# Optimization experiments

Hardware: AMD Instinct MI355X
Metric: run time of the kernel (lower is better)

Reference implementation:

```python
import jax, jax.numpy as jnp
import numpy as np

B, CIN, NH, W, L, K = 16, 64, 64, 32, 4, 5
EPS = 1e-5
FORGET_BIAS = 1.0


def conv(x, w, b=None):
    # x: [B,C,H,W], w: [O,I,k,k] -> SAME padding, stride 1 (NCHW)
    y = jax.lax.conv_general_dilated(x, w, (1, 1), 'SAME',
                                     dimension_numbers=('NCHW', 'OIHW', 'NCHW'))
    if b is not None:
        y = y + b[None, :, None, None]
    return y


def ln(x, g, b):
    # torch LayerNorm([C,W,W]): normalize each sample over (C,H,W)
    m = jnp.mean(x, axis=(1, 2, 3), keepdims=True)
    v = jnp.mean((x - m) ** 2, axis=(1, 2, 3), keepdims=True)
    return (x - m) * jax.lax.rsqrt(v + EPS) * g[None] + b[None]


def attn_channel(q, kv):
    # q: [B,C,W,H], kv: [B,L,C,W,H]
    b, c, w, h = q.shape
    qf = q.reshape(b, c, w * h)                 # [B,C,HW]
    kf = kv.reshape(b, -1, w * h)               # [B,L*C,HW]
    a = jax.nn.softmax(jnp.einsum('bcp,blp->bcl', qf, kf), axis=2)  # [B,C,L*C]
    out = jnp.einsum('bcl,blp->bcp', a, kf)     # [B,C,HW]
    return out.reshape(b, c, w, h)


def attn_spatial(q, kv):
    # q: [B,C,W,H], kv: [B,L,C,W,H]
    b, c, w, h = q.shape
    qf = q.reshape(b, c, w * h).transpose(0, 2, 1)          # [B,HW,C]
    kf = kv.transpose(0, 1, 3, 4, 2).reshape(b, -1, c)      # [B,L*HW,C]
    a = jax.nn.softmax(jnp.einsum('bpc,bqc->bpq', qf, kf), axis=2)  # [B,HW,L*HW]
    out = jnp.einsum('bpq,bqc->bpc', a, kf)                 # [B,HW,C]
    return out.reshape(b, w, h, c).transpose(0, 3, 1, 2)


def setup_inputs() -> dict:
    key = jax.random.key(0)
    ks = iter(jax.random.split(key, 64))
    rn = lambda shape, s=1.0: jax.random.normal(next(ks), shape, jnp.float32) * s
    ones = lambda shape: jnp.ones(shape, jnp.float32)
    zeros = lambda shape: jnp.zeros(shape, jnp.float32)
    s = 0.02
    d = {}
    d['x_t'] = rn((B, CIN, W, W))
    d['h_t'] = rn((B, NH, W, W))
    d['c_t'] = rn((B, NH, W, W))
    d['c_historys'] = rn((B, L, NH, W, W))
    d['m_t'] = rn((B, NH, W, W))
    d['w_x'] = rn((7 * NH, CIN, K, K), s); d['ln_x_g'] = ones((7 * NH, W, W)); d['ln_x_b'] = zeros((7 * NH, W, W))
    d['w_h'] = rn((4 * NH, NH, K, K), s);  d['ln_h_g'] = ones((4 * NH, W, W)); d['ln_h_b'] = zeros((4 * NH, W, W))
    d['w_m'] = rn((3 * NH, NH, K, K), s);  d['ln_m_g'] = ones((3 * NH, W, W)); d['ln_m_b'] = zeros((3 * NH, W, W))
    d['w_o'] = rn((NH, 2 * NH, K, K), s);  d['ln_o_g'] = ones((NH, W, W));     d['ln_o_b'] = zeros((NH, W, W))
    d['w_last'] = rn((NH, 2 * NH, 1, 1), s)
    d['s_norm_g'] = ones((NH, W, W)); d['s_norm_b'] = zeros((NH, W, W))
    d['c_norm_g'] = ones((NH, W, W)); d['c_norm_b'] = zeros((NH, W, W))
    d['ca_w1'] = rn((NH, NH, K, K), s); d['ca_b1'] = zeros((NH,))
    d['ca_ln_g'] = ones((NH, W, W));    d['ca_ln_b'] = zeros((NH, W, W))
    d['ca_w2'] = rn((NH, NH, 1, 1), s); d['ca_b2'] = zeros((NH,))
    d['sa_w1'] = rn((NH, NH, K, K), s)
    d['sa_ln_g'] = ones((NH, W, W));    d['sa_ln_b'] = zeros((NH, W, W))
    d['sa_w2'] = rn((NH, NH, 1, 1), s)
    d['attn_w'] = rn((NH, NH, 1, 1), s)
    return d


def reference(x_t, h_t, c_t, c_historys, m_t,
              w_x, ln_x_g, ln_x_b, w_h, ln_h_g, ln_h_b, w_m, ln_m_g, ln_m_b,
              w_o, ln_o_g, ln_o_b, w_last,
              s_norm_g, s_norm_b, c_norm_g, c_norm_b,
              ca_w1, ca_b1, ca_ln_g, ca_ln_b, ca_w2, ca_b2,
              sa_w1, sa_ln_g, sa_ln_b, sa_w2, attn_w):
    x_concat = ln(conv(x_t, w_x), ln_x_g, ln_x_b)
    h_concat = ln(conv(h_t, w_h), ln_h_g, ln_h_b)
    m_concat = ln(conv(m_t, w_m), ln_m_g, ln_m_b)
    (i_x, f_x, g_x, i_xp, f_xp, g_xp, o_x) = jnp.split(x_concat, 7, axis=1)
    (i_h, f_h, g_h, o_h) = jnp.split(h_concat, 4, axis=1)
    (i_m, f_m, g_m) = jnp.split(m_concat, 3, axis=1)

    i_t = jax.nn.sigmoid(i_x + i_h)
    f_t = jax.nn.sigmoid(f_x + f_h + FORGET_BIAS)
    g_t = jnp.tanh(g_x + g_h)

    # attn_sum_fussion(c_t, query=f_t, keys=c_historys, values=c_historys)
    sp = ln(c_t + attn_spatial(f_t, c_historys), s_norm_g, s_norm_b)
    ch = ln(c_t + attn_channel(f_t, c_historys), c_norm_g, c_norm_b)
    s_a = conv(jax.nn.relu(ln(conv(sp, sa_w1), sa_ln_g, sa_ln_b)), sa_w2)
    c_a = conv(jax.nn.relu(ln(conv(ch, ca_w1, ca_b1), ca_ln_g, ca_ln_b)), ca_w2, ca_b2)
    attn = conv(s_a + c_a, attn_w)
    c_new = attn + i_t * g_t

    i_tp = jax.nn.sigmoid(i_xp + i_m)
    f_tp = jax.nn.sigmoid(f_xp + f_m + FORGET_BIAS)
    g_tp = jnp.tanh(g_xp + g_m)
    m_new = f_tp * m_t + i_tp * g_tp

    mem = jnp.concatenate((c_new, m_new), axis=1)
    o_t = jax.nn.sigmoid(o_x + o_h + ln(conv(mem, w_o), ln_o_g, ln_o_b))
    h_new = o_t * jnp.tanh(conv(mem, w_last))
    return h_new, c_new, m_new
```

## Files before the change

kernel.cpp:

```cpp
#include <hip/hip_runtime.h>
#include <hip/hip_bf16.h>

#define N1 (1u << 20)

typedef __attribute__((ext_vector_type(8))) short s8v;
typedef __attribute__((ext_vector_type(4))) float f4v;

static __device__ __forceinline__ float sigm(float x){ return 1.f/(1.f + __expf(-x)); }
static __device__ __forceinline__ float tanh_(float x){ return 1.f - 2.f/(__expf(2.f*x) + 1.f); }

static __device__ __forceinline__ ushort f2b(float f){
  union { float f; uint u; } x; x.f = f;
  uint r = x.u + 0x7FFFu + ((x.u >> 16) & 1u);
  return (ushort)(r >> 16);
}

static __device__ __forceinline__ void red_atomic2(float s, float q, float* d, int b, int t){
  #pragma unroll
  for (int m = 32; m; m >>= 1){ s += __shfl_xor(s, m); q += __shfl_xor(q, m); }
  if ((t & 63) == 0){ atomicAdd(&d[b*2], s); atomicAdd(&d[b*2+1], q); }
}

__global__ __launch_bounds__(256) void k_pre(
    const float* __restrict__ wX, ushort* __restrict__ dX,
    const float* __restrict__ wH, ushort* __restrict__ dH,
    const float* __restrict__ wM, ushort* __restrict__ dM,
    const float* __restrict__ x_t, ushort* __restrict__ xT,
    const float* __restrict__ h_t, ushort* __restrict__ hT,
    const float* __restrict__ m_t, ushort* __restrict__ mT,
    float* __restrict__ zs)
{
  const int bid = blockIdx.x, t = threadIdx.x;
  __shared__ __align__(16) float T[64][68];
  if (bid < 5600){
    if (bid == 0) zs[t] = 0.f;
    int idx = bid*256 + t;
    const float* s; ushort* d; int Co;
    if (idx < 716800){ s=wX; d=dX; Co=448; }
    else if ((idx -= 716800) < 409600){ s=wH; d=dH; Co=256; }
    else if ((idx -= 409600) < 307200){ s=wM; d=dM; Co=192; }
    else return;
    int ci = idx & 63; int r = idx >> 6; int co = r % Co; int tap = r / Co;
    d[idx] = f2b(s[((size_t)(co*64 + ci))*25 + tap]);
    return;
  }
  const int j = bid - 5600;
  const int p0 = (j & 15) << 6;
  const int lp = j >> 4;
  const float* src; ushort* outT; int pl;
  if (lp < 16){ src = x_t; outT = xT; pl = lp; }
  else if (lp < 32){ src = h_t; outT = hT; pl = lp - 16; }
  else { src = m_t; outT = mT; pl = lp - 32; }
  const float* sp = src + ((size_t)pl << 16);
  const int c = t >> 2, g = t & 3;
  #pragma unroll
  for (int i = 0; i < 4; ++i)
    *(float4*)&T[c][(g<<4)+(i<<2)] = *(const float4*)(sp + ((size_t)c << 10) + p0 + (g<<4) + (i<<2));
  __syncthreads();
  const int p = t >> 2, c0 = (t & 3) << 4;
  uint w4[8];
  #pragma unroll
  for (int k = 0; k < 8; ++k)
    w4[k] = (uint)f2b(T[c0+2*k][p]) | ((uint)f2b(T[c0+2*k+1][p]) << 16);
  ushort* dst = outT + ((((size_t)pl << 10) + p0 + p) << 6) + c0;
  *(uint4*)(dst)     = *(uint4*)&w4[0];
  *(uint4*)(dst + 8) = *(uint4*)&w4[4];
}

__global__ __launch_bounds__(256) void k_postgates(
    const float* __restrict__ wO, ushort* __restrict__ dO,
    const float* __restrict__ wSA, ushort* __restrict__ dSA,
    const float* __restrict__ wCA, ushort* __restrict__ dCA,
    const float* __restrict__ chist, ushort* __restrict__ kvC, ushort* __restrict__ kvT,
    const float* __restrict__ ft, ushort* __restrict__ ftC, ushort* __restrict__ qT,
    const float* __restrict__ memo, ushort* __restrict__ memoT)
{
  const int bid = blockIdx.x, t = threadIdx.x;
  __shared__ __align__(16) float T[64][68];
  if (bid < 1600){
    int idx = bid*256 + t;
    const float* s; ushort* d; int Co, Ci;
    if (idx < 204800){ s=wO; d=dO; Co=64; Ci=128; }
    else if ((idx -= 204800) < 102400){ s=wSA; d=dSA; Co=64; Ci=64; }
    else if ((idx -= 102400) < 102400){ s=wCA; d=dCA; Co=64; Ci=64; }
    else return;
    int ci = idx % Ci; int r = idx / Ci; int co = r % Co; int tap = r / Co;
    d[idx] = f2b(s[((size_t)(co*Ci + ci))*25 + tap]);
    return;
  }
  const int j = bid - 1600;
  const int p0 = (j & 15) << 6;
  const int lp = j >> 4;
  const int c = t >> 2, g = t & 3;
  if (lp < 80){
    const float* src; ushort* outC; ushort* outT; int pl;
    if (lp < 64){ src = chist; outC = kvC; outT = kvT; pl = lp; }
    else { src = ft; outC = ftC; outT = qT; pl = lp - 64; }
    const float* sp = src + ((size_t)pl << 16);
    #pragma unroll
    for (int i = 0; i < 4; ++i){
      float4 f = *(const float4*)(sp + ((size_t)c << 10) + p0 + (g<<4) + (i<<2));
      *(float4*)&T[c][(g<<4)+(i<<2)] = f;
      uint2 pk2;
      pk2.x = (uint)f2b(f.x) | ((uint)f2b(f.y) << 16);
      pk2.y = (uint)f2b(f.z) | ((uint)f2b(f.w) << 16);
      *(uint2*)(outC + ((((size_t)pl << 6) + c) << 10) + p0 + (g<<4) + (i<<2)) = pk2;
    }
    __syncthreads();
    const int p = t >> 2, c0 = (t & 3) << 4;
    uint w4[8];
    #pragma unroll
    for (int k = 0; k < 8; ++k)
      w4[k] = (uint)f2b(T[c0+2*k][p]) | ((uint)f2b(T[c0+2*k+1][p]) << 16);
    ushort* dst = outT + ((((size_t)pl << 10) + p0 + p) << 6) + c0;
    *(uint4*)(dst)     = *(uint4*)&w4[0];
    *(uint4*)(dst + 8) = *(uint4*)&w4[4];
  } else {
    const int b = lp - 80;
    const float* sp = memo + ((size_t)(b*2 + 1) << 16);
    #pragma unroll
    for (int i = 0; i < 4; ++i)
      *(float4*)&T[c][(g<<4)+(i<<2)] = *(const float4*)(sp + ((size_t)c << 10) + p0 + (g<<4) + (i<<2));
    __syncthreads();
    const int p = t >> 2, c0 = (t & 3) << 4;
    uint w4[8];
    #pragma unroll
    for (int k = 0; k < 8; ++k)
      w4[k] = (uint)f2b(T[c0+2*k][p]) | ((uint)f2b(T[c0+2*k+1][p]) << 16);
    ushort* dst = memoT + ((((size_t)b << 10) + p0 + p) << 7) + 64 + c0;
    *(uint4*)(dst)     = *(uint4*)&w4[0];
    *(uint4*)(dst + 8) = *(uint4*)&w4[4];
  }
}

struct PT { const float* s; ushort* d; const float* st; const float* g; const float* bb; };

__global__ __launch_bounds__(256) void k_prepT3(PT ja, PT jb, PT jc, int n0, int n1, float invN)
{
  const int lp = blockIdx.y;
  PT j; int pl;
  if (lp < n0){ j = ja; pl = lp; }
  else if (lp < n0 + n1){ j = jb; pl = lp - n0; }
  else { j = jc; pl = lp - n0 - n1; }
  const float* sp = j.s + ((size_t)pl << 16);
  float mean = 0.f, rstd = 0.f;
  if (j.st){
    float s0 = j.st[pl*2], s1 = j.st[pl*2+1];
    mean = s0*invN; rstd = rsqrtf(s1*invN - mean*mean + 1e-5f);
  }
  const int p0 = blockIdx.x << 6;
  __shared__ __align__(16) float T[64][68];
  const int t = threadIdx.x, c = t >> 2, g4 = t & 3;
  #pragma unroll
  for (int i = 0; i < 4; ++i){
    const int px = (g4 << 4) + (i << 2);
    float4 f = *(const float4*)(sp + ((size_t)c << 10) + p0 + px);
    if (j.st){
      const size_t li = ((size_t)c << 10) + p0 + px;
      float4 gv = *(const float4*)(j.g + li);
      float4 bv = *(const float4*)(j.bb + li);
      f.x = (f.x - mean)*rstd*gv.x + bv.x;
      f.y = (f.y - mean)*rstd*gv.y + bv.y;
      f.z = (f.z - mean)*rstd*gv.z + bv.z;
      f.w = (f.w - mean)*rstd*gv.w + bv.w;
    }
    *(float4*)&T[c][px] = f;
  }
  __syncthreads();
  const int p = t >> 2, c0 = (t & 3) << 4;
  uint w4[8];
  #pragma unroll
  for (int k = 0; k < 8; ++k){
    ushort lo = f2b(T[c0 + 2*k][p]);
    ushort hi = f2b(T[c0 + 2*k + 1][p]);
    w4[k] = (uint)lo | ((uint)hi << 16);
  }
  ushort* dst = j.d + ((((size_t)pl << 10) + p0 + p) << 6) + c0;
  *(uint4*)(dst)     = *(uint4*)&w4[0];
  *(uint4*)(dst + 8) = *(uint4*)&w4[4];
}

struct Seg {
  const ushort* inT; const ushort* w; const float* bias;
  float* out; float* ostat;
  int Cin, Cout;
};
struct Segs3 { Seg s[3]; int b1, b2; };

template<int MT, int RPB>
__global__ __launch_bounds__(256, MT==4 ? 2 : 3) void k_convX(Segs3 Sg)
{
  constexpr int CO   = MT*16;
  constexpr int NW   = 5*CO*4;
  constexpr int ITW  = (NW + 255) / 256;
  constexpr int DXSH = (MT == 4 ? 8 : 7);
  constexpr int PXB  = 32/RPB;
  constexpr int ROWS = RPB + 4;
  constexpr int RPW  = RPB/4;
  constexpr int NTIL = RPB/2;
  constexpr int SUN2 = ROWS*36;

  const int b = blockIdx.y;
  const int cog = blockIdx.x / PXB, pxblk = blockIdx.x % PXB;
  const int si = (cog >= Sg.b1) + (cog >= Sg.b2);
  const Seg sg = Sg.s[si];
  const int base = si == 0 ? 0 : (si == 1 ? Sg.b1 : Sg.b2);
  const int co0 = (cog - base) * CO;
  const int r0 = pxblk * RPB;
  const int t = threadIdx.x, w = t >> 6, l = t & 63;
  const int lane16 = l & 15, quad = l >> 4;

  __shared__ __align__(16) ushort S_[4][ROWS][36][8];
  __shared__ __align__(16) ushort W_[2][5*CO*32];

  f4v acc[MT][NTIL];
  #pragma unroll
  for (int mi = 0; mi < MT; ++mi)
    #pragma unroll
    for (int n = 0; n < NTIL; ++n) acc[mi][n] = (f4v){0.f,0.f,0.f,0.f};

  size_t woff0[ITW];
  #pragma unroll
  for (int it = 0; it < ITW; ++it){
    const int u = t + it*256;
    const int l16u = u & 15, qu = (u >> 4) & 3;
    const int miu = (u >> 6) & (MT - 1), dxu = u >> DXSH;
    woff0[it] = ((size_t)(dxu*sg.Cout + co0 + miu*16 + l16u))*sg.Cin + (qu << 3);
  }
  const size_t wdy = (size_t)5 * sg.Cout * sg.Cin;

  const int ncc = sg.Cin >> 5;
  for (int cc = 0; cc < ncc; ++cc){
    __syncthreads();
    for (int idx = t; idx < SUN2; idx += 256){
      const int row = idx / 36, col = idx - row*36;
      const int ir = r0 - 2 + row, ic = col - 2;
      uint4 pk[4] = {make_uint4(0,0,0,0),make_uint4(0,0,0,0),make_uint4(0,0,0,0),make_uint4(0,0,0,0)};
      if ((unsigned)ir < 32u && (unsigned)ic < 32u){
        const ushort* bp = sg.inT + ((size_t)((b << 10) + (ir << 5) + ic)) * sg.Cin + (cc << 5);
        #pragma unroll
        for (int q = 0; q < 4; ++q) pk[q] = *(const uint4*)(bp + (q << 3));
      }
      #pragma unroll
      for (int q = 0; q < 4; ++q) *(uint4*)&S_[q][row][col][0] = pk[q];
    }
    {
      uint4 wreg[ITW];
      #pragma unroll
      for (int it = 0; it < ITW; ++it)
        if (ITW*256 == NW || t + it*256 < NW)
          wreg[it] = *(const uint4*)(sg.w + woff0[it] + (cc << 5));
      #pragma unroll
      for (int it = 0; it < ITW; ++it)
        if (ITW*256 == NW || t + it*256 < NW)
          *(uint4*)&W_[0][(size_t)(t + it*256) * 8] = wreg[it];
    }
    __syncthreads();
    #pragma unroll
    for (int dy = 0; dy < 5; ++dy){
      uint4 nreg[ITW];
      if (dy < 4){
        #pragma unroll
        for (int it = 0; it < ITW; ++it)
          if (ITW*256 == NW || t + it*256 < NW)
            nreg[it] = *(const uint4*)(sg.w + woff0[it] + (size_t)(dy+1)*wdy + (cc << 5));
      }
      #pragma unroll
      for (int dx = 0; dx < 5; ++dx){
        s8v a[MT];
        #pragma unroll
        for (int mi = 0; mi < MT; ++mi){
          const int au = ((((dx*MT + mi) << 2) + quad) << 4) + lane16;
          a[mi] = *(const s8v*)&W_[dy & 1][au << 3];
        }
        #pragma unroll
        for (int n = 0; n < NTIL; ++n){
          const int srow = w*RPW + (n >> 1) + dy;
          const int col = ((n & 1) << 4) + lane16 + dx;
          s8v bb = *(const s8v*)&S_[quad][srow][col][0];
          #pragma unroll
          for (int mi = 0; mi < MT; ++mi)
            acc[mi][n] = __builtin_amdgcn_mfma_f32_16x16x32_bf16(a[mi], bb, acc[mi][n], 0, 0, 0);
        }
      }
      if (dy < 4){
        #pragma unroll
        for (int it = 0; it < ITW; ++it)
          if (ITW*256 == NW || t + it*256 < NW)
            *(uint4*)&W_[(dy+1) & 1][(size_t)(t + it*256) * 8] = nreg[it];
      }
      __syncthreads();
    }
  }
  float lsum = 0.f, lsq = 0.f;
  #pragma unroll
  for (int mi = 0; mi < MT; ++mi){
    const int co = co0 + mi*16 + (quad << 2);
    #pragma unroll
    for (int n = 0; n < NTIL; ++n){
      const int row = r0 + w*RPW + (n >> 1);
      const int col = ((n & 1) << 4) + lane16;
      #pragma unroll
      for (int i = 0; i < 4; ++i){
        float v = acc[mi][n][i] + (sg.bias ? sg.bias[co+i] : 0.f);
        sg.out[(((size_t)(b*sg.Cout + co + i)) << 10) + (row << 5) + col] = v;
        lsum += v; lsq += v*v;
      }
    }
  }
  if (sg.ostat) red_atomic2(lsum, lsq, sg.ostat, b, t);
}

__global__ __launch_bounds__(256) void k_gates(
    const float* __restrict__ bufx, const float* __restrict__ bufh, const float* __restrict__ bufm,
    const float* __restrict__ lnxg, const float* __restrict__ lnxb,
    const float* __restrict__ lnhg, const float* __restrict__ lnhb,
    const float* __restrict__ lnmg, const float* __restrict__ lnmb,
    const float* __restrict__ m_t, const float* __restrict__ stats,
    float* __restrict__ ft, float* __restrict__ ig, float* __restrict__ osum,
    float* __restrict__ memo, float* __restrict__ out_m)
{
  const int idx = blockIdx.x*256 + threadIdx.x;
  const int b = idx >> 16, rem = idx & 65535;
  const int c = rem >> 10, p = rem & 1023;

  float mx = stats[b*2]      * (1.f/458752.f);
  float vx = stats[b*2+1]    * (1.f/458752.f) - mx*mx;  float rx = rsqrtf(vx + 1e-5f);
  float mh = stats[32+b*2]   * (1.f/262144.f);
  float vh = stats[32+b*2+1] * (1.f/262144.f) - mh*mh;  float rh = rsqrtf(vh + 1e-5f);
  float mm = stats[64+b*2]   * (1.f/196608.f);
  float vm = stats[64+b*2+1] * (1.f/196608.f) - mm*mm;  float rm = rsqrtf(vm + 1e-5f);

  auto LX = [&](int k){
    size_t ch = (size_t)k*64 + c; size_t gi = ((size_t)b*448 + ch)*1024 + p; size_t li = ch*1024 + p;
    return (bufx[gi] - mx)*rx*lnxg[li] + lnxb[li]; };
  auto LH = [&](int k){
    size_t ch = (size_t)k*64 + c; size_t gi = ((size_t)b*256 + ch)*1024 + p; size_t li = ch*1024 + p;
    return (bufh[gi] - mh)*rh*lnhg[li] + lnhb[li]; };
  auto LM = [&](int k){
    size_t ch = (size_t)k*64 + c; size_t gi = ((size_t)b*192 + ch)*1024 + p; size_t li = ch*1024 + p;
    return (bufm[gi] - mm)*rm*lnmg[li] + lnmb[li]; };

  float i_t = sigm(LX(0) + LH(0));
  float f_t = sigm(LX(1) + LH(1) + 1.f);
  float g_t = tanh_(LX(2) + LH(2));
  float i_p = sigm(LX(3) + LM(0));
  float f_p = sigm(LX(4) + LM(1) + 1.f);
  float g_p = tanh_(LX(5) + LM(2));
  float ox = LX(6), oh = LH(3);

  ft[idx]   = f_t;
  ig[idx]   = i_t * g_t;
  osum[idx] = ox + oh;
  float mn = f_p * m_t[idx] + i_p * g_p;
  out_m[idx] = mn;
  memo[((size_t)(b*128 + 64 + c) << 10) + p] = mn;
}

__global__ __launch_bounds__(256) void k_spat_chlog(
    const ushort* __restrict__ qT, const ushort* __restrict__ kvC, const ushort* __restrict__ kvT,
    float* __restrict__ num, float* __restrict__ den,
    const ushort* __restrict__ ftC, float* __restrict__ lg)
{
  __shared__ __align__(16) char smem[44288];
  const int bid = blockIdx.x, t = threadIdx.x;
  const int w = t >> 6, l = t & 63;
  const int lane16 = l & 15, quad = l >> 4;

  if (bid < 512){
    const int p0 = (bid & 15) << 6, b = (bid >> 4) & 15, half = bid >> 8;
    ushort (*Kt)[72] = reinterpret_cast<ushort(*)[72]>(smem);
    ushort (*Kc)[72] = reinterpret_cast<ushort(*)[72]>(smem + 9216);
    ushort (*Eb)[72] = reinterpret_cast<ushort(*)[72]>(smem + 18432);
    float  (*XO)[65] = reinterpret_cast<float(*)[65]>(smem + 27648);

    s8v qa0, qa1;
    {
      const ushort* qr = qT + ((((size_t)b << 10) + p0 + (w << 4) + lane16) << 6) + (quad << 3);
      qa0 = *(const s8v*)(qr);
      qa1 = *(const s8v*)(qr + 32);
    }
    f4v o0 = {0.f,0.f,0.f,0.f}, o1 = o0, o2 = o0, o3 = o0, dacc = o0;
    const short oneb = (short)0x3F80;
    const s8v ones = { oneb, oneb, oneb, oneb, oneb, oneb, oneb, oneb };

    const int r = t >> 2, g4 = (t & 3) << 4;
    for (int ck = 0; ck < 32; ++ck){
      const int chunk = (half << 5) + ck;
      const int lidx = chunk >> 4, pk = (chunk & 15) << 6;
      __syncthreads();
      {
        const ushort* sc = kvC + ((((size_t)(b*4 + lidx) << 6) + r) << 10) + pk + g4;
        *(uint4*)&Kc[r][g4]     = *(const uint4*)(sc);
        *(uint4*)&Kc[r][g4 + 8] = *(const uint4*)(sc + 8);
        const ushort* st = kvT + ((((size_t)(b*4 + lidx) << 10) + pk + r) << 6) + g4;
        *(uint4*)&Kt[r][g4]     = *(const uint4*)(st);
        *(uint4*)&Kt[r][g4 + 8] = *(const uint4*)(st + 8);
      }
      __syncthreads();
      #pragma unroll
      for (int nt = 0; nt < 4; ++nt){
        const ushort* bt = &Kt[(nt << 4) + lane16][quad << 3];
        s8v b0 = *(const s8v*)(bt);
        s8v b1 = *(const s8v*)(bt + 32);
        f4v s = {0.f,0.f,0.f,0.f};
        s = __builtin_amdgcn_mfma_f32_16x16x32_bf16(qa0, b0, s, 0, 0, 0);
        s = __builtin_amdgcn_mfma_f32_16x16x32_bf16(qa1, b1, s, 0, 0, 0);
        #pragma unroll
        for (int i = 0; i < 4; ++i){
          float e = __expf(s[i] - 12.f);
          Eb[(w << 4) + (quad << 2) + i][(nt << 4) + lane16] = f2b(e);
        }
      }
      __syncthreads();
      #pragma unroll
      for (int ks = 0; ks < 2; ++ks){
        s8v ea = *(const s8v*)&Eb[(w << 4) + lane16][(ks << 5) + (quad << 3)];
        dacc = __builtin_amdgcn_mfma_f32_16x16x32_bf16(ea, ones, dacc, 0, 0, 0);
        s8v bc0 = *(const s8v*)&Kc[ 0 + lane16][(ks << 5) + (quad << 3)];
        s8v bc1 = *(const s8v*)&Kc[16 + lane16][(ks << 5) + (quad << 3)];
        s8v bc2 = *(const s8v*)&Kc[32 + lane16][(ks << 5) + (quad << 3)];
        s8v bc3 = *(const s8v*)&Kc[48 + lane16][(ks << 5) + (quad << 3)];
        o0 = __builtin_amdgcn_mfma_f32_16x16x32_bf16(ea, bc0, o0, 0, 0, 0);
        o1 = __builtin_amdgcn_mfma_f32_16x16x32_bf16(ea, bc1, o1, 0, 0, 0);
        o2 = __builtin_amdgcn_mfma_f32_16x16x32_bf16(ea, bc2, o2, 0, 0, 0);
        o3 = __builtin_amdgcn_mfma_f32_16x16x32_bf16(ea, bc3, o3, 0, 0, 0);
      }
    }
    {
      const int pxl = (w << 4) + (quad << 2);
      if (lane16 == 0){
        float* dp = den + (((size_t)(half*16 + b)) << 10) + p0 + pxl;
        dp[0] = dacc[0]; dp[1] = dacc[1]; dp[2] = dacc[2]; dp[3] = dacc[3];
      }
      XO[ 0 + lane16][pxl+0] = o0[0]; XO[ 0 + lane16][pxl+1] = o0[1];
      XO[ 0 + lane16][pxl+2] = o0[2]; XO[ 0 + lane16][pxl+3] = o0[3];
      XO[16 + lane16][pxl+0] = o1[0]; XO[16 + lane16][pxl+1] = o1[1];
      XO[16 + lane16][pxl+2] = o1[2]; XO[16 + lane16][pxl+3] = o1[3];
      XO[32 + lane16][pxl+0] = o2[0]; XO[32 + lane16][pxl+1] = o2[1];
      XO[32 + lane16][pxl+2] = o2[2]; XO[32 + lane16][pxl+3] = o2[3];
      XO[48 + lane16][pxl+0] = o3[0]; XO[48 + lane16][pxl+1] = o3[1];
      XO[48 + lane16][pxl+2] = o3[2]; XO[48 + lane16][pxl+3] = o3[3];
    }
    __syncthreads();
    {
      const int ch = t >> 2;
      float* nout = num + (size_t)half * N1;
      #pragma unroll
      for (int i = 0; i < 4; ++i){
        size_t gi = ((size_t)b << 16) + ((size_t)ch << 10) + p0 + g4 + (i << 2);
        float4 ov;
        ov.x = XO[ch][g4 + (i << 2) + 0];
        ov.y = XO[ch][g4 + (i << 2) + 1];
        ov.z = XO[ch][g4 + (i << 2) + 2];
        ov.w = XO[ch][g4 + (i << 2) + 3];
        *(float4*)(nout + gi) = ov;
      }
    }
  } else {
    const int j = bid - 512;
    const int bx = j & 7, b = j >> 3;
    const int np = bx >> 1, mp = bx & 1;
    ushort (*As)[32][8] = reinterpret_cast<ushort(*)[32][8]>(smem);
    ushort (*Bs)[64][8] = reinterpret_cast<ushort(*)[64][8]>(smem + 4096);
    f4v acc[2];
    acc[0] = (f4v){0.f,0.f,0.f,0.f}; acc[1] = (f4v){0.f,0.f,0.f,0.f};

    for (int kc = 0; kc < 16; ++kc){
      __syncthreads();
      {
        const int c = t >> 3, q = t & 7;
        *(uint4*)&As[q][c][0] = *(const uint4*)(ftC + (((size_t)(b*64 + mp*32 + c)) << 10) + (kc<<6) + (q<<3));
      }
      #pragma unroll
      for (int it = 0; it < 2; ++it){
        const int idx = t + it*256;
        const int r2 = idx >> 3, q = idx & 7;
        *(uint4*)&Bs[q][r2][0] = *(const uint4*)(kvC + ((((size_t)(b*4 + np) << 6) + r2) << 10) + (kc<<6) + (q<<3));
      }
      __syncthreads();
      #pragma unroll
      for (int ks = 0; ks < 2; ++ks){
        s8v a0 = *(const s8v*)&As[(ks<<2)+quad][lane16][0];
        s8v a1 = *(const s8v*)&As[(ks<<2)+quad][16 + lane16][0];
        s8v bb = *(const s8v*)&Bs[(ks<<2)+quad][(w<<4) + lane16][0];
        acc[0] = __builtin_amdgcn_mfma_f32_16x16x32_bf16(a0, bb, acc[0], 0, 0, 0);
        acc[1] = __builtin_amdgcn_mfma_f32_16x16x32_bf16(a1, bb, acc[1], 0, 0, 0);
      }
    }
    #pragma unroll
    for (int mi = 0; mi < 2; ++mi)
      #pragma unroll
      for (int i = 0; i < 4; ++i){
        const int c = mp*32 + mi*16 + (quad<<2) + i;
        const int n = (np<<6) + (w<<4) + lane16;
        lg[(((size_t)(b*64 + c)) << 8) + n] = acc[mi][i];
      }
  }
}

__global__ __launch_bounds__(256) void k_chsm_spcomb(
    const float* __restrict__ a, ushort* __restrict__ ab,
    const float* __restrict__ num, const float* __restrict__ den,
    const float* __restrict__ c_t, float* __restrict__ sp_raw, float* __restrict__ stats)
{
  const int bid = blockIdx.x, t = threadIdx.x;
  if (bid < 256){
    const int row  = bid*4 + (t >> 6);
    const int lane = t & 63;
    const float* rp = a + ((size_t)row << 8);
    float v0 = rp[lane], v1 = rp[lane+64], v2 = rp[lane+128], v3 = rp[lane+192];
    float mx = fmaxf(fmaxf(v0, v1), fmaxf(v2, v3));
    #pragma unroll
    for (int m = 32; m; m >>= 1) mx = fmaxf(mx, __shfl_xor(mx, m));
    v0 = __expf(v0 - mx); v1 = __expf(v1 - mx); v2 = __expf(v2 - mx); v3 = __expf(v3 - mx);
    float s = v0 + v1 + v2 + v3;
    #pragma unroll
    for (int m = 32; m; m >>= 1) s += __shfl_xor(s, m);
    float inv = 1.f / s;
    ushort* op = ab + ((size_t)row << 8);
    op[lane] = f2b(v0*inv); op[lane+64] = f2b(v1*inv);
    op[lane+128] = f2b(v2*inv); op[lane+192] = f2b(v3*inv);
  } else {
    const int j = bid - 256;
    const int p0 = (j & 15) << 6, b = j >> 4;
    const int ch = t >> 2, g4 = (t & 3) << 4;
    float lsum = 0.f, lsq = 0.f;
    #pragma unroll
    for (int i = 0; i < 4; ++i){
      const int px = p0 + g4 + (i << 2);
      size_t gi = ((size_t)b << 16) + ((size_t)ch << 10) + px;
      float4 n0 = *(const float4*)(num + gi);
      float4 n1 = *(const float4*)(num + (size_t)N1 + gi);
      const float* d0 = den + (((size_t)b) << 10) + px;
      const float* d1 = den + (((size_t)(16 + b)) << 10) + px;
      float4 cv = *(const float4*)(c_t + gi);
      float4 ov;
      ov.x = cv.x + (n0.x + n1.x) / (d0[0] + d1[0]);
      ov.y = cv.y + (n0.y + n1.y) / (d0[1] + d1[1]);
      ov.z = cv.z + (n0.z + n1.z) / (d0[2] + d1[2]);
      ov.w = cv.w + (n0.w + n1.w) / (d0[3] + d1[3]);
      *(float4*)(sp_raw + gi) = ov;
      lsum += ov.x + ov.y + ov.z + ov.w;
      lsq  += ov.x*ov.x + ov.y*ov.y + ov.z*ov.z + ov.w*ov.w;
    }
    red_atomic2(lsum, lsq, stats, b, t);
  }
}

__global__ __launch_bounds__(256) void k_chout_m(
    const ushort* __restrict__ chlb, const ushort* __restrict__ kvT,
    const float* __restrict__ c_t, float* __restrict__ ch_raw, float* __restrict__ stats)
{
  const int p0 = blockIdx.x << 6, b = blockIdx.y;
  const int t = threadIdx.x, w = t >> 6, l = t & 63;
  const int lane16 = l & 15, quad = l >> 4;
  __shared__ __align__(16) ushort As[32][64][8];
  __shared__ __align__(16) ushort Bs[32][32][8];
  #pragma unroll
  for (int it = 0; it < 8; ++it){
    const int idx = t + it*256;
    const int c = idx >> 5, q = idx & 31;
    *(uint4*)&As[q][c][0] = *(const uint4*)(chlb + (((size_t)(b*64 + c)) << 8) + (q<<3));
  }
  __syncthreads();
  s8v a[8];
  #pragma unroll
  for (int ks = 0; ks < 8; ++ks)
    a[ks] = *(const s8v*)&As[(ks<<2)+quad][(w<<4) + lane16][0];
  float lsum = 0.f, lsq = 0.f;
  for (int pc = 0; pc < 2; ++pc){
    __syncthreads();
    #pragma unroll
    for (int it = 0; it < 4; ++it){
      const int idx = t + it*256;
      const int px = idx >> 5, q = idx & 31;
      const int plane = (b<<2) + (q>>3);
      *(uint4*)&Bs[q][px][0] = *(const uint4*)(kvT + ((((size_t)plane << 10) + p0 + (pc<<5) + px) << 6) + ((q&7)<<3));
    }
    __syncthreads();
    #pragma unroll
    for (int nt = 0; nt < 2; ++nt){
      f4v o = {0.f,0.f,0.f,0.f};
      #pragma unroll
      for (int ks = 0; ks < 8; ++ks){
        s8v bb = *(const s8v*)&Bs[(ks<<2)+quad][(nt<<4) + lane16][0];
        o = __builtin_amdgcn_mfma_f32_16x16x32_bf16(a[ks], bb, o, 0, 0, 0);
      }
      #pragma unroll
      for (int i = 0; i < 4; ++i){
        const int c = (w<<4) + (quad<<2) + i;
        const int px = p0 + (pc<<5) + (nt<<4) + lane16;
        size_t gi = ((size_t)b << 16) + ((size_t)c << 10) + px;
        float v = c_t[gi] + o[i];
        ch_raw[gi] = v;
        lsum += v; lsq += v*v;
      }
    }
  }
  red_atomic2(lsum, lsq, stats, b, t);
}

__global__ __launch_bounds__(256) void k_attnfinal(
    const float* __restrict__ samid, const float* __restrict__ camid,
    const float* __restrict__ stats_sa, const float* __restrict__ stats_ca,
    const float* __restrict__ salng, const float* __restrict__ salnb,
    const float* __restrict__ calng, const float* __restrict__ calnb,
    const float* __restrict__ wsa2, const float* __restrict__ wca2,
    const float* __restrict__ cab2, const float* __restrict__ wat,
    const float* __restrict__ ig, float* __restrict__ out_c, float* __restrict__ memo,
    ushort* __restrict__ memoT)
{
  const int p0 = blockIdx.x << 6, b = blockIdx.y, t = threadIdx.x;
  const int tc = t & 15, tp = t >> 4;
  __shared__ __align__(16) float R[64][68];
  __shared__ __align__(16) float Wl[64][68];
  __shared__ __align__(16) float Ms[64][68];
  const float invN = 1.f/65536.f;
  float acc[4][4] = {};
  #pragma unroll
  for (int pass = 0; pass < 2; ++pass){
    const float* mid = pass ? camid : samid;
    const float* st  = pass ? stats_ca : stats_sa;
    const float* g   = pass ? calng : salng;
    const float* bb  = pass ? calnb : salnb;
    const float* w   = pass ? wca2  : wsa2;
    float mean = st[b*2]*invN;
    float var  = st[b*2+1]*invN - mean*mean;
    float rstd = rsqrtf(var + 1e-5f);
    __syncthreads();
    {
      const int j = t & 63, c0 = t >> 6;
      for (int ci = c0; ci < 64; ci += 4){
        size_t gi = ((size_t)b << 16) + ((size_t)ci << 10) + p0 + j;
        size_t li = ((size_t)ci << 10) + p0 + j;
        float v = (mid[gi] - mean)*rstd*g[li] + bb[li];
        R[ci][j] = fmaxf(v, 0.f);
      }
      const int ci2 = t & 63, c20 = t >> 6;
      for (int c2 = c20; c2 < 64; c2 += 4) Wl[ci2][c2] = w[((size_t)c2 << 6) + ci2];
    }
    __syncthreads();
    for (int ci = 0; ci < 64; ++ci){
      float wv[4], rv[4];
      *(float4*)wv = *(const float4*)&Wl[ci][4*tc];
      *(float4*)rv = *(const float4*)&R[ci][4*tp];
      #pragma unroll
      for (int i = 0; i < 4; ++i)
        #pragma unroll
        for (int j = 0; j < 4; ++j)
          acc[i][j] = fmaf(wv[i], rv[j], acc[i][j]);
    }
  }
  {
    float b2[4];
    #pragma unroll
    for (int i = 0; i < 4; ++i) b2[i] = cab2[4*tc + i];
    #pragma unroll
    for (int i = 0; i < 4; ++i)
      #pragma unroll
      for (int j = 0; j < 4; ++j)
        Ms[4*tc+i][4*tp+j] = acc[i][j] + b2[i];
  }
  __syncthreads();
  {
    const int ci2 = t & 63, c20 = t >> 6;
    for (int c2 = c20; c2 < 64; c2 += 4) Wl[ci2][c2] = wat[((size_t)c2 << 6) + ci2];
  }
  __syncthreads();
  float acc2[4][4] = {};
  for (int c2 = 0; c2 < 64; ++c2){
    float wv[4], mv[4];
    *(float4*)wv = *(const float4*)&Wl[c2][4*tc];
    *(float4*)mv = *(const float4*)&Ms[c2][4*tp];
    #pragma unroll
    for (int i = 0; i < 4; ++i)
      #pragma unroll
      for (int j = 0; j < 4; ++j)
        acc2[i][j] = fmaf(wv[i], mv[j], acc2[i][j]);
  }
  float vv[4][4];
  #pragma unroll
  for (int i = 0; i < 4; ++i)
    #pragma unroll
    for (int j = 0; j < 4; ++j){
      size_t gi = ((size_t)b << 16) + ((size_t)(4*tc + i) << 10) + p0 + 4*tp + j;
      float v = acc2[i][j] + ig[gi];
      vv[i][j] = v;
      out_c[gi] = v;
      memo[((size_t)(b*128 + 4*tc + i) << 10) + p0 + 4*tp + j] = v;
    }
  #pragma unroll
  for (int j = 0; j < 4; ++j){
    uint2 pk;
    pk.x = (uint)f2b(vv[0][j]) | ((uint)f2b(vv[1][j]) << 16);
    pk.y = (uint)f2b(vv[2][j]) | ((uint)f2b(vv[3][j]) << 16);
    *(uint2*)(memoT + ((((size_t)b << 10) + p0 + 4*tp + j) << 7) + 4*tc) = pk;
  }
}

__global__ __launch_bounds__(256) void k_final(
    const float* __restrict__ memo, const float* __restrict__ wlast,
    const float* __restrict__ bufo, const float* __restrict__ osum,
    const float* __restrict__ stats_o, const float* __restrict__ lnog, const float* __restrict__ lnob,
    float* __restrict__ out_h)
{
  const int p0 = blockIdx.x << 6, b = blockIdx.y, t = threadIdx.x;
  const int tc = t & 15, tp = t >> 4;
  __shared__ __align__(16) float Msh[64][68];
  __shared__ __align__(16) float Wt[64][68];
  float acc[4][4] = {};
  #pragma unroll
  for (int half = 0; half < 2; ++half){
    __syncthreads();
    {
      const int j = t & 63, c0 = t >> 6;
      for (int ci = c0; ci < 64; ci += 4)
        Msh[ci][j] = memo[((size_t)(b*128 + half*64 + ci) << 10) + p0 + j];
      const int ci2 = t & 63, co0 = t >> 6;
      for (int co = co0; co < 64; co += 4) Wt[ci2][co] = wlast[((size_t)co << 7) + half*64 + ci2];
    }
    __syncthreads();
    for (int ci = 0; ci < 64; ++ci){
      float wv[4], mv[4];
      *(float4*)wv = *(const float4*)&Wt[ci][4*tc];
      *(float4*)mv = *(const float4*)&Msh[ci][4*tp];
      #pragma unroll
      for (int i = 0; i < 4; ++i)
        #pragma unroll
        for (int j = 0; j < 4; ++j)
          acc[i][j] = fmaf(wv[i], mv[j], acc[i][j]);
    }
  }
  float mean = stats_o[b*2]*(1.f/65536.f);
  float var  = stats_o[b*2+1]*(1.f/65536.f) - mean*mean;
  float rstd = rsqrtf(var + 1e-5f);
  #pragma unroll
  for (int i = 0; i < 4; ++i)
    #pragma unroll
    for (int j = 0; j < 4; ++j){
      const int co = 4*tc + i, p = p0 + 4*tp + j;
      size_t gi = ((size_t)b << 16) + ((size_t)co << 10) + p;
      size_t li = ((size_t)co << 10) + p;
      float lno = (bufo[gi] - mean)*rstd*lnog[li] + lnob[li];
      float o = sigm(osum[gi] + lno);
      out_h[gi] = o * tanh_(acc[i][j]);
    }
}

extern "C" void kernel_launch(void* const* d_in, const int* in_sizes, int n_in,
                              void* d_out, int out_size, void* d_ws, size_t ws_size,
                              hipStream_t stream)
{
  const float* x_t   = (const float*)d_in[0];
  const float* h_t   = (const float*)d_in[1];
  const float* c_t   = (const float*)d_in[2];
  const float* chist = (const float*)d_in[3];
  const float* m_t   = (const float*)d_in[4];
  const float* w_x   = (const float*)d_in[5];
  const float* lnxg  = (const float*)d_in[6];
  const float* lnxb  = (const float*)d_in[7];
  const float* w_h   = (const float*)d_in[8];
  const float* lnhg  = (const float*)d_in[9];
  const float* lnhb  = (const float*)d_in[10];
  const float* w_m   = (const float*)d_in[11];
  const float* lnmg  = (const float*)d_in[12];
  const float* lnmb  = (const float*)d_in[13];
  const float* w_o   = (const float*)d_in[14];
  const float* lnog  = (const float*)d_in[15];
  const float* lnob  = (const float*)d_in[16];
  const float* w_last= (const float*)d_in[17];
  const float* sng   = (const float*)d_in[18];
  const float* snb   = (const float*)d_in[19];
  const float* cng   = (const float*)d_in[20];
  const float* cnb   = (const float*)d_in[21];
  const float* ca_w1 = (const float*)d_in[22];
  const float* ca_b1 = (const float*)d_in[23];
  const float* calng = (const float*)d_in[24];
  const float* calnb = (const float*)d_in[25];
  const float* ca_w2 = (const float*)d_in[26];
  const float* ca_b2 = (const float*)d_in[27];
  const float* sa_w1 = (const float*)d_in[28];
  const float* salng = (const float*)d_in[29];
  const float* salnb = (const float*)d_in[30];
  const float* sa_w2 = (const float*)d_in[31];
  const float* attn_w= (const float*)d_in[32];

  float* out = (float*)d_out;
  float* ws  = (float*)d_ws;

  float* stats = ws;
  float* bufx  = ws + 1024;
  float* bufh  = bufx + 7*(size_t)N1;
  float* bufm  = bufh + 4*(size_t)N1;
  float* ft    = bufm + 3*(size_t)N1;
  float* ig    = ft   + (size_t)N1;
  float* osum  = ig   + (size_t)N1;
  float* memo  = osum + (size_t)N1;
  float* sp    = bufx;
  float* ch    = bufx + (size_t)N1;
  float* samid = bufx + 2*(size_t)N1;
  float* camid = bufx + 3*(size_t)N1;
  float* bufo  = bufx + 4*(size_t)N1;
  float* chl   = bufx + 5*(size_t)N1;
  ushort* kvC  = (ushort*)bufh;
  ushort* kvT  = kvC + 4*(size_t)N1;
  ushort* qT   = (ushort*)bufm;
  ushort* ftC  = qT + (size_t)N1;

  ushort* xT   = (ushort*)memo;
  ushort* hT   = xT + (size_t)N1;
  ushort* mT   = hT + (size_t)N1;
  ushort* spT  = ftC + (size_t)N1;
  ushort* chT  = spT + (size_t)N1;
  ushort* memoT = chT + (size_t)N1;
  float*  numB = bufx;

  ushort* wbx = (ushort*)ft;
  ushort* wbh = wbx + 716800;
  ushort* wbm = wbh + 409600;
  ushort* wbo  = (ushort*)(chl + 262144);
  ushort* wbsa = wbo + 204800;
  ushort* wbca = wbsa + 102400;
  ushort* chlb = wbca + 102400;
  float*  denP = chl + 600000;

  float* out_h = out;
  float* out_c = out + (size_t)N1;
  float* out_m = out + 2*(size_t)N1;

  k_pre<<<dim3(6368), dim3(256), 0, stream>>>(w_x, wbx, w_h, wbh, w_m, wbm,
                                              x_t, xT, h_t, hT, m_t, mT, stats);

  {
    Segs3 XHM;
    XHM.s[0] = Seg{ xT, wbx, nullptr, bufx, stats+0,  64, 448 };
    XHM.s[1] = Seg{ hT, wbh, nullptr, bufh, stats+32, 64, 256 };
    XHM.s[2] = Seg{ mT, wbm, nullptr, bufm, stats+64, 64, 192 };
    XHM.b1 = 7; XHM.b2 = 11;
    k_convX<4,8><<<dim3(56,16), dim3(256), 0, stream>>>(XHM);
  }

  k_gates<<<dim3(4096), dim3(256), 0, stream>>>(bufx, bufh, bufm, lnxg, lnxb, lnhg, lnhb,
                                                lnmg, lnmb, m_t, stats,
                                                ft, ig, osum, memo, out_m);

  k_postgates<<<dim3(3136), dim3(256), 0, stream>>>(w_o, wbo, sa_w1, wbsa, ca_w1, wbca,
                                                    chist, kvC, kvT, ft, ftC, qT,
                                                    memo, memoT);

  k_spat_chlog<<<dim3(640), dim3(256), 0, stream>>>(qT, kvC, kvT, numB, denP, ftC, chl);

  k_chsm_spcomb<<<dim3(512), dim3(256), 0, stream>>>(chl, chlb, numB, denP, c_t, sp, stats+96);

  k_chout_m<<<dim3(16,16), dim3(256), 0, stream>>>(chlb, kvT, c_t, ch, stats+128);

  {
    PT js{ sp, spT, stats+96,  sng, snb };
    PT jc{ ch, chT, stats+128, cng, cnb };
    k_prepT3<<<dim3(16,32), dim3(256), 0, stream>>>(js, jc, js, 16, 16, 1.f/65536.f);
  }

  {
    Segs3 SC;
    SC.s[0] = Seg{ spT, wbsa, nullptr, samid, stats+160, 64, 64 };
    SC.s[1] = Seg{ chT, wbca, ca_b1,   camid, stats+192, 64, 64 };
    SC.s[2] = SC.s[1];
    SC.b1 = 2; SC.b2 = 1000;
    k_convX<2,8><<<dim3(16,16), dim3(256), 0, stream>>>(SC);
  }

  k_attnfinal<<<dim3(16,16), dim3(256), 0, stream>>>(samid, camid, stats+160, stats+192,
                                                     salng, salnb, calng, calnb,
                                                     sa_w2, ca_w2, ca_b2, attn_w,
                                                     ig, out_c, memo, memoT);

  {
    Segs3 O;
    O.s[0] = Seg{ memoT, wbo, nullptr, bufo, stats+224, 128, 64 };
    O.s[1] = O.s[0]; O.s[2] = O.s[0];
    O.b1 = 1000; O.b2 = 1000;
    k_convX<2,8><<<dim3(8,16), dim3(256), 0, stream>>>(O);
  }

  k_final<<<dim3(16,16), dim3(256), 0, stream>>>(memo, w_last, bufo, osum, stats+224,
                                                 lnog, lnob, out_h);
}
```

Measured before the change: 471.2 us.

## Repack weights and activations into conv-tile-contiguous blocked layouts

```diff
diff --git a/kernel.cpp b/kernel.cpp
--- a/kernel.cpp
+++ b/kernel.cpp
@@ -19,6 +19,24 @@
   #pragma unroll
   for (int m = 32; m; m >>= 1){ s += __shfl_xor(s, m); q += __shfl_xor(q, m); }
   if ((t & 63) == 0){ atomicAdd(&d[b*2], s); atomicAdd(&d[b*2+1], q); }
+}
+
+static __device__ __forceinline__ void wpack1(const float* __restrict__ s,
+                                              ushort* __restrict__ d,
+                                              int idx, int Co, int Ci, int CO)
+{
+  const int MTl = CO >> 4;
+  const int NWl = 20*CO;
+  const int nCot = Co / CO;
+  int e = idx & 7; int r = idx >> 3;
+  int u = r % NWl; r /= NWl;
+  int cot = r % nCot; r /= nCot;
+  int dy = r % 5; int cc = r / 5;
+  int l16 = u & 15, q = (u >> 4) & 3, t2 = u >> 6;
+  int mi = t2 % MTl, dx = t2 / MTl;
+  int co = cot*CO + mi*16 + l16;
+  int ci = (cc << 5) + (q << 3) + e;
+  d[idx] = f2b(s[((size_t)(co*Ci + ci))*25 + dy*5 + dx]);
 }
 
 __global__ __launch_bounds__(256) void k_pre(
@@ -35,13 +53,9 @@
   if (bid < 5600){
     if (bid == 0) zs[t] = 0.f;
     int idx = bid*256 + t;
-    const float* s; ushort* d; int Co;
-    if (idx < 716800){ s=wX; d=dX; Co=448; }
-    else if ((idx -= 716800) < 409600){ s=wH; d=dH; Co=256; }
-    else if ((idx -= 409600) < 307200){ s=wM; d=dM; Co=192; }
-    else return;
-    int ci = idx & 63; int r = idx >> 6; int co = r % Co; int tap = r / Co;
-    d[idx] = f2b(s[((size_t)(co*64 + ci))*25 + tap]);
+    if (idx < 716800){ wpack1(wX, dX, idx, 448, 64, 64); }
+    else if ((idx -= 716800) < 409600){ wpack1(wH, dH, idx, 256, 64, 64); }
+    else if ((idx -= 409600) < 307200){ wpack1(wM, dM, idx, 192, 64, 64); }
     return;
   }
   const int j = bid - 5600;
@@ -62,9 +76,11 @@
   #pragma unroll
   for (int k = 0; k < 8; ++k)
     w4[k] = (uint)f2b(T[c0+2*k][p]) | ((uint)f2b(T[c0+2*k+1][p]) << 16);
-  ushort* dst = outT + ((((size_t)pl << 10) + p0 + p) << 6) + c0;
-  *(uint4*)(dst)     = *(uint4*)&w4[0];
-  *(uint4*)(dst + 8) = *(uint4*)&w4[4];
+  const int q0 = c0 >> 3;
+  ushort* d0 = outT + ((((size_t)pl*8 + q0    ) << 10) + p0 + p)*8;
+  ushort* d1 = outT + ((((size_t)pl*8 + q0 + 1) << 10) + p0 + p)*8;
+  *(uint4*)d0 = *(uint4*)&w4[0];
+  *(uint4*)d1 = *(uint4*)&w4[4];
 }
 
 __global__ __launch_bounds__(256) void k_postgates(
@@ -79,13 +95,9 @@
   __shared__ __align__(16) float T[64][68];
   if (bid < 1600){
     int idx = bid*256 + t;
-    const float* s; ushort* d; int Co, Ci;
-    if (idx < 204800){ s=wO; d=dO; Co=64; Ci=128; }
-    else if ((idx -= 204800) < 102400){ s=wSA; d=dSA; Co=64; Ci=64; }
-    else if ((idx -= 102400) < 102400){ s=wCA; d=dCA; Co=64; Ci=64; }
-    else return;
-    int ci = idx % Ci; int r = idx / Ci; int co = r % Co; int tap = r / Co;
-    d[idx] = f2b(s[((size_t)(co*Ci + ci))*25 + tap]);
+    if (idx < 204800){ wpack1(wO, dO, idx, 64, 128, 32); }
+    else if ((idx -= 204800) < 102400){ wpack1(wSA, dSA, idx, 64, 64, 32); }
+    else if ((idx -= 102400) < 102400){ wpack1(wCA, dCA, idx, 64, 64, 32); }
     return;
   }
   const int j = bid - 1600;
@@ -127,9 +139,11 @@
     #pragma unroll
     for (int k = 0; k < 8; ++k)
       w4[k] = (uint)f2b(T[c0+2*k][p]) | ((uint)f2b(T[c0+2*k+1][p]) << 16);
-    ushort* dst = memoT + ((((size_t)b << 10) + p0 + p) << 7) + 64 + c0;
-    *(uint4*)(dst)     = *(uint4*)&w4[0];
-    *(uint4*)(dst + 8) = *(uint4*)&w4[4];
+    const int q0 = 8 + (c0 >> 3);
+    ushort* d0 = memoT + ((((size_t)(b*16 + q0    )) << 10) + p0 + p)*8;
+    ushort* d1 = memoT + ((((size_t)(b*16 + q0 + 1)) << 10) + p0 + p)*8;
+    *(uint4*)d0 = *(uint4*)&w4[0];
+    *(uint4*)d1 = *(uint4*)&w4[4];
   }
 }
 
@@ -175,9 +189,11 @@
     ushort hi = f2b(T[c0 + 2*k + 1][p]);
     w4[k] = (uint)lo | ((uint)hi << 16);
   }
-  ushort* dst = j.d + ((((size_t)pl << 10) + p0 + p) << 6) + c0;
-  *(uint4*)(dst)     = *(uint4*)&w4[0];
-  *(uint4*)(dst + 8) = *(uint4*)&w4[4];
+  const int q0 = c0 >> 3;
+  ushort* d0 = j.d + ((((size_t)pl*8 + q0    ) << 10) + p0 + p)*8;
+  ushort* d1 = j.d + ((((size_t)pl*8 + q0 + 1) << 10) + p0 + p)*8;
+  *(uint4*)d0 = *(uint4*)&w4[0];
+  *(uint4*)d1 = *(uint4*)&w4[4];
 }
 
 struct Seg {
@@ -193,77 +209,72 @@
   constexpr int CO   = MT*16;
   constexpr int NW   = 5*CO*4;
   constexpr int ITW  = (NW + 255) / 256;
-  constexpr int DXSH = (MT == 4 ? 8 : 7);
   constexpr int PXB  = 32/RPB;
   constexpr int ROWS = RPB + 4;
   constexpr int RPW  = RPB/4;
   constexpr int NTIL = RPB/2;
-  constexpr int SUN2 = ROWS*36;
+  constexpr int SUN  = 4*ROWS*36;
 
   const int b = blockIdx.y;
   const int cog = blockIdx.x / PXB, pxblk = blockIdx.x % PXB;
   const int si = (cog >= Sg.b1) + (cog >= Sg.b2);
   const Seg sg = Sg.s[si];
   const int base = si == 0 ? 0 : (si == 1 ? Sg.b1 : Sg.b2);
-  const int co0 = (cog - base) * CO;
+  const int cot = cog - base;
+  const int co0 = cot * CO;
   const int r0 = pxblk * RPB;
   const int t = threadIdx.x, w = t >> 6, l = t & 63;
   const int lane16 = l & 15, quad = l >> 4;
+  const int nCot = sg.Cout / CO;
+  const int ngrp = sg.Cin >> 3;
 
   __shared__ __align__(16) ushort S_[4][ROWS][36][8];
-  __shared__ __align__(16) ushort W_[2][5*CO*32];
+  __shared__ __align__(16) ushort W_[2][NW*8];
 
   f4v acc[MT][NTIL];
   #pragma unroll
   for (int mi = 0; mi < MT; ++mi)
     #pragma unroll
     for (int n = 0; n < NTIL; ++n) acc[mi][n] = (f4v){0.f,0.f,0.f,0.f};
-
-  size_t woff0[ITW];
-  #pragma unroll
-  for (int it = 0; it < ITW; ++it){
-    const int u = t + it*256;
-    const int l16u = u & 15, qu = (u >> 4) & 3;
-    const int miu = (u >> 6) & (MT - 1), dxu = u >> DXSH;
-    woff0[it] = ((size_t)(dxu*sg.Cout + co0 + miu*16 + l16u))*sg.Cin + (qu << 3);
-  }
-  const size_t wdy = (size_t)5 * sg.Cout * sg.Cin;
 
   const int ncc = sg.Cin >> 5;
   for (int cc = 0; cc < ncc; ++cc){
     __syncthreads();
-    for (int idx = t; idx < SUN2; idx += 256){
-      const int row = idx / 36, col = idx - row*36;
+    for (int idx = t; idx < SUN; idx += 256){
+      const int q   = idx / (ROWS*36);
+      const int rem = idx - q*(ROWS*36);
+      const int row = rem / 36, col = rem - row*36;
       const int ir = r0 - 2 + row, ic = col - 2;
-      uint4 pk[4] = {make_uint4(0,0,0,0),make_uint4(0,0,0,0),make_uint4(0,0,0,0),make_uint4(0,0,0,0)};
-      if ((unsigned)ir < 32u && (unsigned)ic < 32u){
-        const ushort* bp = sg.inT + ((size_t)((b << 10) + (ir << 5) + ic)) * sg.Cin + (cc << 5);
-        #pragma unroll
-        for (int q = 0; q < 4; ++q) pk[q] = *(const uint4*)(bp + (q << 3));
-      }
-      #pragma unroll
-      for (int q = 0; q < 4; ++q) *(uint4*)&S_[q][row][col][0] = pk[q];
+      uint4 pk = make_uint4(0,0,0,0);
+      if ((unsigned)ir < 32u && (unsigned)ic < 32u)
+        pk = *(const uint4*)(sg.inT + ((((size_t)(b*ngrp + (cc<<2) + q)) << 10) + (ir<<5) + ic)*8);
+      *(uint4*)&S_[q][row][col][0] = pk;
     }
     {
+      const ushort* wb = sg.w + ((((size_t)(cc*5)*nCot + cot)*NW) << 3);
       uint4 wreg[ITW];
       #pragma unroll
-      for (int it = 0; it < ITW; ++it)
-        if (ITW*256 == NW || t + it*256 < NW)
-          wreg[it] = *(const uint4*)(sg.w + woff0[it] + (cc << 5));
-      #pragma unroll
-      for (int it = 0; it < ITW; ++it)
-        if (ITW*256 == NW || t + it*256 < NW)
-          *(uint4*)&W_[0][(size_t)(t + it*256) * 8] = wreg[it];
+      for (int it = 0; it < ITW; ++it){
+        const int u = t + it*256;
+        if (ITW*256 == NW || u < NW) wreg[it] = *(const uint4*)(wb + ((size_t)u << 3));
+      }
+      #pragma unroll
+      for (int it = 0; it < ITW; ++it){
+        const int u = t + it*256;
+        if (ITW*256 == NW || u < NW) *(uint4*)&W_[0][(size_t)u * 8] = wreg[it];
+      }
     }
     __syncthreads();
     #pragma unroll
     for (int dy = 0; dy < 5; ++dy){
       uint4 nreg[ITW];
       if (dy < 4){
+        const ushort* wbn = sg.w + ((((size_t)(cc*5 + dy + 1)*nCot + cot)*NW) << 3);
         #pragma unroll
-        for (int it = 0; it < ITW; ++it)
-          if (ITW*256 == NW || t + it*256 < NW)
-            nreg[it] = *(const uint4*)(sg.w + woff0[it] + (size_t)(dy+1)*wdy + (cc << 5));
+        for (int it = 0; it < ITW; ++it){
+          const int u = t + it*256;
+          if (ITW*256 == NW || u < NW) nreg[it] = *(const uint4*)(wbn + ((size_t)u << 3));
+        }
       }
       #pragma unroll
       for (int dx = 0; dx < 5; ++dx){
@@ -285,9 +296,10 @@
       }
       if (dy < 4){
         #pragma unroll
-        for (int it = 0; it < ITW; ++it)
-          if (ITW*256 == NW || t + it*256 < NW)
-            *(uint4*)&W_[(dy+1) & 1][(size_t)(t + it*256) * 8] = nreg[it];
+        for (int it = 0; it < ITW; ++it){
+          const int u = t + it*256;
+          if (ITW*256 == NW || u < NW) *(uint4*)&W_[(dy+1) & 1][(size_t)u * 8] = nreg[it];
+        }
       }
       __syncthreads();
     }
@@ -695,7 +707,8 @@
     uint2 pk;
     pk.x = (uint)f2b(vv[0][j]) | ((uint)f2b(vv[1][j]) << 16);
     pk.y = (uint)f2b(vv[2][j]) | ((uint)f2b(vv[3][j]) << 16);
-    *(uint2*)(memoT + ((((size_t)b << 10) + p0 + 4*tp + j) << 7) + 4*tc) = pk;
+    const int px = p0 + 4*tp + j;
+    *(uint2*)(memoT + ((((size_t)(b*16 + (tc >> 1))) << 10) + px)*8 + ((tc & 1) << 2)) = pk;
   }
 }
 
```

Result: no change. 476.0 us (+1.0%).

## Single-buffer conv weight tile with register prefetch to raise occupancy

Applied to the files above, without the earlier changes.

```diff
diff --git a/kernel.cpp b/kernel.cpp
--- a/kernel.cpp
+++ b/kernel.cpp
@@ -188,7 +188,7 @@
 struct Segs3 { Seg s[3]; int b1, b2; };
 
 template<int MT, int RPB>
-__global__ __launch_bounds__(256, MT==4 ? 2 : 3) void k_convX(Segs3 Sg)
+__global__ __launch_bounds__(256, MT==4 ? 3 : 4) void k_convX(Segs3 Sg)
 {
   constexpr int CO   = MT*16;
   constexpr int NW   = 5*CO*4;
@@ -211,7 +211,7 @@
   const int lane16 = l & 15, quad = l >> 4;
 
   __shared__ __align__(16) ushort S_[4][ROWS][36][8];
-  __shared__ __align__(16) ushort W_[2][5*CO*32];
+  __shared__ __align__(16) ushort W_[NW*8];
 
   f4v acc[MT][NTIL];
   #pragma unroll
@@ -229,7 +229,26 @@
   }
   const size_t wdy = (size_t)5 * sg.Cout * sg.Cin;
 
+  uint4 wreg[ITW];
+  auto loadW = [&](int cc_, int dy_){
+    #pragma unroll
+    for (int it = 0; it < ITW; ++it){
+      const int u = t + it*256;
+      if (ITW*256 == NW || u < NW)
+        wreg[it] = *(const uint4*)(sg.w + woff0[it] + (size_t)dy_*wdy + (cc_ << 5));
+    }
+  };
+  auto writeW = [&](){
+    #pragma unroll
+    for (int it = 0; it < ITW; ++it){
+      const int u = t + it*256;
+      if (ITW*256 == NW || u < NW)
+        *(uint4*)&W_[(size_t)u * 8] = wreg[it];
+    }
+  };
+
   const int ncc = sg.Cin >> 5;
+  loadW(0, 0);
   for (int cc = 0; cc < ncc; ++cc){
     __syncthreads();
     for (int idx = t; idx < SUN2; idx += 256){
@@ -244,34 +263,18 @@
       #pragma unroll
       for (int q = 0; q < 4; ++q) *(uint4*)&S_[q][row][col][0] = pk[q];
     }
-    {
-      uint4 wreg[ITW];
-      #pragma unroll
-      for (int it = 0; it < ITW; ++it)
-        if (ITW*256 == NW || t + it*256 < NW)
-          wreg[it] = *(const uint4*)(sg.w + woff0[it] + (cc << 5));
-      #pragma unroll
-      for (int it = 0; it < ITW; ++it)
-        if (ITW*256 == NW || t + it*256 < NW)
-          *(uint4*)&W_[0][(size_t)(t + it*256) * 8] = wreg[it];
-    }
+    writeW();
+    loadW(cc, 1);
     __syncthreads();
     #pragma unroll
     for (int dy = 0; dy < 5; ++dy){
-      uint4 nreg[ITW];
-      if (dy < 4){
-        #pragma unroll
-        for (int it = 0; it < ITW; ++it)
-          if (ITW*256 == NW || t + it*256 < NW)
-            nreg[it] = *(const uint4*)(sg.w + woff0[it] + (size_t)(dy+1)*wdy + (cc << 5));
-      }
       #pragma unroll
       for (int dx = 0; dx < 5; ++dx){
         s8v a[MT];
         #pragma unroll
         for (int mi = 0; mi < MT; ++mi){
           const int au = ((((dx*MT + mi) << 2) + quad) << 4) + lane16;
-          a[mi] = *(const s8v*)&W_[dy & 1][au << 3];
+          a[mi] = *(const s8v*)&W_[au << 3];
         }
         #pragma unroll
         for (int n = 0; n < NTIL; ++n){
@@ -284,12 +287,12 @@
         }
       }
       if (dy < 4){
-        #pragma unroll
-        for (int it = 0; it < ITW; ++it)
-          if (ITW*256 == NW || t + it*256 < NW)
-            *(uint4*)&W_[(dy+1) & 1][(size_t)(t + it*256) * 8] = nreg[it];
-      }
-      __syncthreads();
+        __syncthreads();
+        writeW();
+        if (dy < 3) loadW(cc, dy + 2);
+        else if (cc + 1 < ncc) loadW(cc + 1, 0);
+        __syncthreads();
+      }
     }
   }
   float lsum = 0.f, lsq = 0.f;
```

Result: slower. 502.5 us (+6.6%).
